# Kernel tuning notes

Measured on AMD Instinct MI355X. Metric: run time of the kernel, lower is better.

## Reference

```python
import jax, jax.numpy as jnp
import numpy as np

CUTOFF = 0.5


def setup_inputs() -> dict:
    key = jax.random.key(0)
    k_z, k_d, k_w, k_mu, k_sg = jax.random.split(key, 5)
    N, D_IN, D_OUT = 8192, 128, 128
    z = jax.random.normal(k_z, (N, D_IN), dtype=jnp.float32)
    dist_matrix = jax.random.uniform(k_d, (N, N), dtype=jnp.float32)
    W = jax.random.normal(k_w, (D_IN, D_OUT), dtype=jnp.float32)
    B = jnp.zeros((D_OUT,), dtype=jnp.float32)
    mu = jax.random.normal(k_mu, (1,), dtype=jnp.float32)
    sigma = jax.random.normal(k_sg, (1,), dtype=jnp.float32)
    return {"z": z, "dist_matrix": dist_matrix, "W": W, "B": B, "mu": mu, "sigma": sigma}


def reference(z, dist_matrix, W, B, mu, sigma):
    N = dist_matrix.shape[0]
    # transform every source node once: h[j] = z[j] @ W + B   [N, D_OUT]
    h = z @ W + B
    # pair mask: within cutoff and i != j
    mask = (dist_matrix < CUTOFF) & (~jnp.eye(N, dtype=bool))
    # safe distance to avoid inf/nan where masked out (original skips those pairs)
    r = jnp.where(mask, dist_matrix, 1.0)
    sens = jnp.exp(-(1.0 / r - 1.0 / mu[0]) ** 2 / (2.0 * sigma[0] ** 2))
    S = jnp.where(mask, sens, 0.0)  # [N, N]
    # z_inter[i] = sum_j S[i, j] * h[j]
    return S @ h
```

## Files before the change

### kernel.cpp

```cpp
#include <hip/hip_runtime.h>
#include <hip/hip_bf16.h>

#define NN 8192
#define DD 128
#define BM 16

typedef __attribute__((ext_vector_type(4))) float f32x4;
typedef __attribute__((ext_vector_type(8))) short bf16x8;

__device__ __forceinline__ unsigned short f2bf(float x) {
    unsigned u = __float_as_uint(x);
    u += 0x7fffu + ((u >> 16) & 1u);
    return (unsigned short)(u >> 16);
}

__global__ void __launch_bounds__(256) h_transform(
    const float* __restrict__ z, const float* __restrict__ W,
    const float* __restrict__ Bv, unsigned short* __restrict__ hT) {
    __shared__ float zs[BM * DD];
    __shared__ float wt[DD * 132];
    const int t = threadIdx.x;
    const int j0 = blockIdx.x * BM;

    {
        const f32x4* zsrc = (const f32x4*)(z + (size_t)j0 * DD);
        f32x4* zdst = (f32x4*)zs;
        zdst[t] = zsrc[t];
        zdst[t + 256] = zsrc[t + 256];
    }
    for (int q = t; q < DD * 32; q += 256) {
        int k = q >> 5;
        int n0 = (q & 31) << 2;
        f32x4 wv = *(const f32x4*)(W + k * DD + n0);
        wt[(n0 + 0) * 132 + k] = wv[0];
        wt[(n0 + 1) * 132 + k] = wv[1];
        wt[(n0 + 2) * 132 + k] = wv[2];
        wt[(n0 + 3) * 132 + k] = wv[3];
    }
    __syncthreads();

    const int n = t >> 1;
    const int ja = (t & 1) << 3;
    float acc[8];
    float bn = Bv[n];
#pragma unroll
    for (int e = 0; e < 8; e++) acc[e] = bn;

#pragma unroll 8
    for (int k4 = 0; k4 < 32; ++k4) {
        f32x4 wv = *(const f32x4*)&wt[n * 132 + (k4 << 2)];
#pragma unroll
        for (int e = 0; e < 8; e++) {
            f32x4 zv = *(const f32x4*)&zs[(ja + e) * DD + (k4 << 2)];
            acc[e] += zv[0] * wv[0] + zv[1] * wv[1] + zv[2] * wv[2] + zv[3] * wv[3];
        }
    }

    const int j = j0 + ja;
    unsigned short* dst = hT + (size_t)n * NN + j;
    uint4 uv;
    uv.x = (unsigned)f2bf(acc[0]) | ((unsigned)f2bf(acc[1]) << 16);
    uv.y = (unsigned)f2bf(acc[2]) | ((unsigned)f2bf(acc[3]) << 16);
    uv.z = (unsigned)f2bf(acc[4]) | ((unsigned)f2bf(acc[5]) << 16);
    uv.w = (unsigned)f2bf(acc[6]) | ((unsigned)f2bf(acc[7]) << 16);
    *(uint4*)dst = uv;
}

__device__ __forceinline__ bf16x8 sfrag(f32x4 a, f32x4 b, int jbase, int diag,
                                        float inv_mu, float ninv2s2) {
    float v0[4] = {a[0], a[1], a[2], a[3]};
    float v1[4] = {b[0], b[1], b[2], b[3]};
    unsigned short h[8];
#pragma unroll
    for (int e = 0; e < 4; ++e) {
        float d = v0[e];
        float q = __builtin_amdgcn_rcpf(d) - inv_mu;
        float s = __expf(q * q * ninv2s2);
        bool keep = (d < 0.5f) & ((jbase + e) != diag);
        h[e] = f2bf(keep ? s : 0.0f);
    }
#pragma unroll
    for (int e = 0; e < 4; ++e) {
        float d = v1[e];
        float q = __builtin_amdgcn_rcpf(d) - inv_mu;
        float s = __expf(q * q * ninv2s2);
        bool keep = (d < 0.5f) & ((jbase + 4 + e) != diag);
        h[4 + e] = f2bf(keep ? s : 0.0f);
    }
    uint4 u;
    u.x = (unsigned)h[0] | ((unsigned)h[1] << 16);
    u.y = (unsigned)h[2] | ((unsigned)h[3] << 16);
    u.z = (unsigned)h[4] | ((unsigned)h[5] << 16);
    u.w = (unsigned)h[6] | ((unsigned)h[7] << 16);
    return __builtin_bit_cast(bf16x8, u);
}

__global__ void __launch_bounds__(64) fused_interact(
    const float* __restrict__ dist, const unsigned short* __restrict__ hT,
    const float* __restrict__ mu, const float* __restrict__ sigma,
    float* __restrict__ outp, float* __restrict__ part, int ksplit) {
    const int l = threadIdx.x;
    const int rt = blockIdx.x / ksplit;
    const int ks = blockIdx.x - rt * ksplit;
    const int klen = NN / ksplit;
    const int kbeg = ks * klen;

    const int row = l & 15;
    const int kc8 = (l >> 4) << 3;
    const int r0 = rt * 32;

    const float inv_mu = 1.0f / mu[0];
    const float sg = sigma[0];
    const float ninv2s2 = -1.0f / (2.0f * sg * sg);

    const float* dp0 = dist + (size_t)(r0 + row) * NN + kc8;
    const float* dp1 = dp0 + (size_t)16 * NN;
    const unsigned short* hp = hT + (size_t)row * NN + kc8;
    const int diag0 = r0 + row;
    const int diag1 = diag0 + 16;

    f32x4 acc[2][8];
#pragma unroll
    for (int m = 0; m < 2; ++m)
#pragma unroll
        for (int f = 0; f < 8; ++f) acc[m][f] = (f32x4){0.f, 0.f, 0.f, 0.f};

    f32x4 dA0a, dA0b, dA1a, dA1b, dB0a, dB0b, dB1a, dB1b;
    uint4 hA[8], hB[8];

#define LOADD(Da, Db, Dc, Dd, H, K)                                          \
    do {                                                                     \
        Da = *(const f32x4*)(dp0 + (K));                                     \
        Db = *(const f32x4*)(dp0 + (K) + 4);                                 \
        Dc = *(const f32x4*)(dp1 + (K));                                     \
        Dd = *(const f32x4*)(dp1 + (K) + 4);                                 \
        _Pragma("unroll") for (int f = 0; f < 8; ++f)                        \
            H[f] = *(const uint4*)(hp + (size_t)f * 16 * NN + (K));          \
    } while (0)

#define COMPUTE(Da, Db, Dc, Dd, H, K)                                        \
    do {                                                                     \
        bf16x8 a0 = sfrag(Da, Db, (K) + kc8, diag0, inv_mu, ninv2s2);        \
        bf16x8 a1 = sfrag(Dc, Dd, (K) + kc8, diag1, inv_mu, ninv2s2);        \
        _Pragma("unroll") for (int f = 0; f < 8; ++f) {                      \
            bf16x8 bb = __builtin_bit_cast(bf16x8, H[f]);                    \
            acc[0][f] = __builtin_amdgcn_mfma_f32_16x16x32_bf16(             \
                a0, bb, acc[0][f], 0, 0, 0);                                 \
            acc[1][f] = __builtin_amdgcn_mfma_f32_16x16x32_bf16(             \
                a1, bb, acc[1][f], 0, 0, 0);                                 \
        }                                                                    \
    } while (0)

    int k = kbeg;
    LOADD(dA0a, dA0b, dA1a, dA1b, hA, k);
    LOADD(dB0a, dB0b, dB1a, dB1b, hB, k + 32);
    const int nt = klen >> 5;
    for (int it = 0; it < nt; it += 2) {
        COMPUTE(dA0a, dA0b, dA1a, dA1b, hA, k);
        if (it + 2 < nt) LOADD(dA0a, dA0b, dA1a, dA1b, hA, k + 64);
        COMPUTE(dB0a, dB0b, dB1a, dB1b, hB, k + 32);
        if (it + 3 < nt) LOADD(dB0a, dB0b, dB1a, dB1b, hB, k + 96);
        k += 64;
    }

    float* po = (ksplit == 1) ? outp : (part + (size_t)ks * (NN * DD));
    const int orow = r0 + ((l >> 4) << 2);
    const int ocol = l & 15;
#pragma unroll
    for (int m = 0; m < 2; ++m)
#pragma unroll
        for (int f = 0; f < 8; ++f)
#pragma unroll
            for (int rr = 0; rr < 4; ++rr)
                po[(size_t)(orow + m * 16 + rr) * DD + f * 16 + ocol] =
                    acc[m][f][rr];
}

__global__ void __launch_bounds__(256) reduce_part(
    const float* __restrict__ part, float* __restrict__ outp, int ksplit) {
    const size_t idx = ((size_t)blockIdx.x * 256 + threadIdx.x) << 2;
    f32x4 s = *(const f32x4*)(part + idx);
    for (int ksp = 1; ksp < ksplit; ++ksp)
        s += *(const f32x4*)(part + (size_t)ksp * (NN * DD) + idx);
    *(f32x4*)(outp + idx) = s;
}

extern "C" void kernel_launch(void* const* d_in, const int* in_sizes, int n_in,
                              void* d_out, int out_size, void* d_ws, size_t ws_size,
                              hipStream_t stream) {
    const float* z = (const float*)d_in[0];
    const float* dist = (const float*)d_in[1];
    const float* W = (const float*)d_in[2];
    const float* Bv = (const float*)d_in[3];
    const float* mu = (const float*)d_in[4];
    const float* sigma = (const float*)d_in[5];
    float* out = (float*)d_out;

    unsigned short* hT = (unsigned short*)d_ws;
    const size_t hT_bytes = (size_t)DD * NN * 2;
    const size_t part_bytes = (size_t)NN * DD * 4;
    float* part = (float*)((char*)d_ws + hT_bytes);

    int ksplit = 1;
    if (ws_size >= hT_bytes + 4 * part_bytes) ksplit = 4;
    else if (ws_size >= hT_bytes + 2 * part_bytes) ksplit = 2;

    h_transform<<<NN / BM, 256, 0, stream>>>(z, W, Bv, hT);
    fused_interact<<<(NN / 32) * ksplit, 64, 0, stream>>>(dist, hT, mu, sigma,
                                                          out, part, ksplit);
    if (ksplit > 1)
        reduce_part<<<(NN * DD) / 1024, 256, 0, stream>>>(part, out, ksplit);
}
```

Measured before the change: 132.6 us.

## Stage hT tiles in shared memory and share across 8 waves per block

The interaction kernel now uses 512-thread blocks (8 waves covering 256 rows) that cooperatively load 512-column chunks of hT into padded LDS. All waves then read their MFMA B operands from LDS, so the global/L2 reads of hT are no longer repeated per wave. The K dimension is split into a fixed 8 slices with a mandatory partial-sum reduction. This assumes the workspace can hold 8 partial buffers, removes the ws_size check, and adds barrier stalls plus a larger reduction pass.

Result: faster. 108.6 us (-18.1%).

```diff
diff --git a/kernel.cpp b/kernel.cpp
--- a/kernel.cpp
+++ b/kernel.cpp
@@ -4,6 +4,11 @@
 #define NN 8192
 #define DD 128
 #define BM 16
+#define JS 8
+#define RPB 256
+#define JSLICE 1024
+#define JCHUNK 512
+#define LSTR 1040
 
 typedef __attribute__((ext_vector_type(4))) float f32x4;
 typedef __attribute__((ext_vector_type(8))) short bf16x8;
@@ -95,19 +100,22 @@
     return __builtin_bit_cast(bf16x8, u);
 }
 
-__global__ void __launch_bounds__(64) fused_interact(
+__global__ void __launch_bounds__(512, 2) fused_interact(
     const float* __restrict__ dist, const unsigned short* __restrict__ hT,
     const float* __restrict__ mu, const float* __restrict__ sigma,
-    float* __restrict__ outp, float* __restrict__ part, int ksplit) {
-    const int l = threadIdx.x;
-    const int rt = blockIdx.x / ksplit;
-    const int ks = blockIdx.x - rt * ksplit;
-    const int klen = NN / ksplit;
-    const int kbeg = ks * klen;
-
+    float* __restrict__ part) {
+    __shared__ uint4 hs4[DD * (LSTR / 16)];
+    char* hs = (char*)hs4;
+
+    const int t = threadIdx.x;
+    const int w = t >> 6;
+    const int l = t & 63;
+    const int rb = blockIdx.x >> 3;
+    const int js = blockIdx.x & 7;
+    const int r0 = rb * RPB + w * 32;
     const int row = l & 15;
     const int kc8 = (l >> 4) << 3;
-    const int r0 = rt * 32;
+    const int q16 = (l >> 4) << 4;
 
     const float inv_mu = 1.0f / mu[0];
     const float sg = sigma[0];
@@ -115,9 +123,9 @@
 
     const float* dp0 = dist + (size_t)(r0 + row) * NN + kc8;
     const float* dp1 = dp0 + (size_t)16 * NN;
-    const unsigned short* hp = hT + (size_t)row * NN + kc8;
     const int diag0 = r0 + row;
     const int diag1 = diag0 + 16;
+    const char* hbase = hs + row * LSTR + q16;
 
     f32x4 acc[2][8];
 #pragma unroll
@@ -126,24 +134,21 @@
         for (int f = 0; f < 8; ++f) acc[m][f] = (f32x4){0.f, 0.f, 0.f, 0.f};
 
     f32x4 dA0a, dA0b, dA1a, dA1b, dB0a, dB0b, dB1a, dB1b;
-    uint4 hA[8], hB[8];
-
-#define LOADD(Da, Db, Dc, Dd, H, K)                                          \
+
+#define LOADD(Da, Db, Dc, Dd, K)                                             \
     do {                                                                     \
         Da = *(const f32x4*)(dp0 + (K));                                     \
         Db = *(const f32x4*)(dp0 + (K) + 4);                                 \
         Dc = *(const f32x4*)(dp1 + (K));                                     \
         Dd = *(const f32x4*)(dp1 + (K) + 4);                                 \
-        _Pragma("unroll") for (int f = 0; f < 8; ++f)                        \
-            H[f] = *(const uint4*)(hp + (size_t)f * 16 * NN + (K));          \
     } while (0)
 
-#define COMPUTE(Da, Db, Dc, Dd, H, K)                                        \
+#define COMPUTE(Da, Db, Dc, Dd, K, LK)                                       \
     do {                                                                     \
         bf16x8 a0 = sfrag(Da, Db, (K) + kc8, diag0, inv_mu, ninv2s2);        \
         bf16x8 a1 = sfrag(Dc, Dd, (K) + kc8, diag1, inv_mu, ninv2s2);        \
         _Pragma("unroll") for (int f = 0; f < 8; ++f) {                      \
-            bf16x8 bb = __builtin_bit_cast(bf16x8, H[f]);                    \
+            bf16x8 bb = *(const bf16x8*)(hbase + f * (16 * LSTR) + (LK));    \
             acc[0][f] = __builtin_amdgcn_mfma_f32_16x16x32_bf16(             \
                 a0, bb, acc[0][f], 0, 0, 0);                                 \
             acc[1][f] = __builtin_amdgcn_mfma_f32_16x16x32_bf16(             \
@@ -151,19 +156,43 @@
         }                                                                    \
     } while (0)
 
-    int k = kbeg;
-    LOADD(dA0a, dA0b, dA1a, dA1b, hA, k);
-    LOADD(dB0a, dB0b, dB1a, dB1b, hB, k + 32);
-    const int nt = klen >> 5;
-    for (int it = 0; it < nt; it += 2) {
-        COMPUTE(dA0a, dA0b, dA1a, dA1b, hA, k);
-        if (it + 2 < nt) LOADD(dA0a, dA0b, dA1a, dA1b, hA, k + 64);
-        COMPUTE(dB0a, dB0b, dB1a, dB1b, hB, k + 32);
-        if (it + 3 < nt) LOADD(dB0a, dB0b, dB1a, dB1b, hB, k + 96);
-        k += 64;
-    }
-
-    float* po = (ksplit == 1) ? outp : (part + (size_t)ks * (NN * DD));
+#pragma unroll 1
+    for (int chunk = 0; chunk < 2; ++chunk) {
+        const int jc = js * JSLICE + chunk * JCHUNK;
+        __syncthreads();
+        {
+            uint4 tmp[16];
+#pragma unroll
+            for (int i = 0; i < 16; ++i) {
+                int c = i * 512 + t;
+                int n = c >> 6;
+                int cb = c & 63;
+                tmp[i] = *(const uint4*)(hT + (size_t)n * NN + jc + cb * 8);
+            }
+#pragma unroll
+            for (int i = 0; i < 16; ++i) {
+                int c = i * 512 + t;
+                int n = c >> 6;
+                int cb = c & 63;
+                *(uint4*)(hs + n * LSTR + cb * 16) = tmp[i];
+            }
+        }
+        __syncthreads();
+
+        LOADD(dA0a, dA0b, dA1a, dA1b, jc);
+        LOADD(dB0a, dB0b, dB1a, dB1b, jc + 32);
+#pragma unroll 1
+        for (int it = 0; it < 16; it += 2) {
+            const int kg = jc + (it << 5);
+            const int lk = it << 6;
+            COMPUTE(dA0a, dA0b, dA1a, dA1b, kg, lk);
+            if (it + 2 < 16) LOADD(dA0a, dA0b, dA1a, dA1b, kg + 64);
+            COMPUTE(dB0a, dB0b, dB1a, dB1b, kg + 32, lk + 64);
+            if (it + 3 < 16) LOADD(dB0a, dB0b, dB1a, dB1b, kg + 96);
+        }
+    }
+
+    float* po = part + (size_t)js * (NN * DD);
     const int orow = r0 + ((l >> 4) << 2);
     const int ocol = l & 15;
 #pragma unroll
@@ -174,13 +203,16 @@
             for (int rr = 0; rr < 4; ++rr)
                 po[(size_t)(orow + m * 16 + rr) * DD + f * 16 + ocol] =
                     acc[m][f][rr];
+#undef LOADD
+#undef COMPUTE
 }
 
 __global__ void __launch_bounds__(256) reduce_part(
-    const float* __restrict__ part, float* __restrict__ outp, int ksplit) {
+    const float* __restrict__ part, float* __restrict__ outp) {
     const size_t idx = ((size_t)blockIdx.x * 256 + threadIdx.x) << 2;
     f32x4 s = *(const f32x4*)(part + idx);
-    for (int ksp = 1; ksp < ksplit; ++ksp)
+#pragma unroll
+    for (int ksp = 1; ksp < JS; ++ksp)
         s += *(const f32x4*)(part + (size_t)ksp * (NN * DD) + idx);
     *(f32x4*)(outp + idx) = s;
 }
@@ -198,16 +230,10 @@
 
     unsigned short* hT = (unsigned short*)d_ws;
     const size_t hT_bytes = (size_t)DD * NN * 2;
-    const size_t part_bytes = (size_t)NN * DD * 4;
     float* part = (float*)((char*)d_ws + hT_bytes);
 
-    int ksplit = 1;
-    if (ws_size >= hT_bytes + 4 * part_bytes) ksplit = 4;
-    else if (ws_size >= hT_bytes + 2 * part_bytes) ksplit = 2;
-
     h_transform<<<NN / BM, 256, 0, stream>>>(z, W, Bv, hT);
-    fused_interact<<<(NN / 32) * ksplit, 64, 0, stream>>>(dist, hT, mu, sigma,
-                                                          out, part, ksplit);
-    if (ksplit > 1)
-        reduce_part<<<(NN * DD) / 1024, 256, 0, stream>>>(part, out, ksplit);
-}
+    fused_interact<<<(NN / RPB) * JS, 512, 0, stream>>>(dist, hT, mu, sigma,
+                                                        part);
+    reduce_part<<<(NN * DD) / 1024, 256, 0, stream>>>(part, out);
+}
```
